# Kernel optimization log

Hardware: AMD Instinct MI355X
Metric: run time of the kernel (lower is better)

## Reference

```python
import jax, jax.numpy as jnp
import numpy as np

EPS = 1e-7
B, F, C, H, W, D = 2, 2, 64, 32, 104, 96


def _pix_homog(h, w):
    ys, xs = jnp.meshgrid(jnp.arange(h, dtype=jnp.float32),
                          jnp.arange(w, dtype=jnp.float32), indexing='ij')
    return jnp.stack([xs.ravel(), ys.ravel(), jnp.ones(h * w, jnp.float32)], 0)  # [3, H*W]


def setup_inputs() -> dict:
    key = jax.random.key(0)
    k1, k2 = jax.random.split(key)
    current_feats = jax.random.normal(k1, (B, C, H, W), jnp.float32)
    lookup_feats = jax.random.normal(k2, (B, F, C, H, W), jnp.float32)

    rng = np.random.RandomState(0)
    # intrinsics at matching (feature) resolution, monodepth2-style
    Km = np.eye(4, dtype=np.float32)
    Km[0, 0] = 0.58 * W
    Km[1, 1] = 1.92 * H
    Km[0, 2] = 0.5 * W
    Km[1, 2] = 0.5 * H
    K = np.tile(Km[None], (B, 1, 1))
    invK = np.linalg.inv(K).astype(np.float32)

    # near-identity relative poses (small rotation perturbation + small translation)
    poses = np.tile(np.eye(4, dtype=np.float32)[None, None], (B, F, 1, 1))
    poses[:, :, :3, :3] += 0.02 * rng.randn(B, F, 3, 3).astype(np.float32)
    poses[:, :, :3, 3] = 0.1 * rng.randn(B, F, 3).astype(np.float32)

    depth_bins = jnp.linspace(0.1, 20.0, D, dtype=jnp.float32)
    return {
        'current_feats': current_feats,
        'lookup_feats': lookup_feats,
        'poses': jnp.asarray(poses),
        'K': jnp.asarray(K),
        'invK': jnp.asarray(invK),
        'depth_bins': depth_bins,
    }


def _grid_sample_zeros(lfT, gx, gy, h, w):
    """Bilinear grid_sample, align_corners=True, padding_mode='zeros'.
    lfT: [B,F,H,W,C]; gx,gy: [B,F,D,H,W] in pixel coords. -> [B,F,D,H,W,C]"""
    x0 = jnp.floor(gx)
    y0 = jnp.floor(gy)
    x0i = x0.astype(jnp.int32)
    y0i = y0.astype(jnp.int32)
    wx1 = gx - x0
    wy1 = gy - y0
    wx0 = 1.0 - wx1
    wy0 = 1.0 - wy1
    bb = jnp.arange(lfT.shape[0])[:, None, None, None, None]
    ff = jnp.arange(lfT.shape[1])[None, :, None, None, None]

    def corner(yi, xi, wgt):
        m = ((xi >= 0) & (xi < w) & (yi >= 0) & (yi < h)).astype(lfT.dtype)
        xc = jnp.clip(xi, 0, w - 1)
        yc = jnp.clip(yi, 0, h - 1)
        v = lfT[bb, ff, yc, xc]                      # [B,F,D,H,W,C]
        return v * (m * wgt)[..., None]

    return (corner(y0i, x0i, wy0 * wx0) + corner(y0i, x0i + 1, wy0 * wx1)
            + corner(y0i + 1, x0i, wy1 * wx0) + corner(y0i + 1, x0i + 1, wy1 * wx1))


def reference(current_feats, lookup_feats, poses, K, invK, depth_bins):
    b, c, h, w = current_feats.shape
    f = lookup_feats.shape[1]
    d = depth_bins.shape[0]

    # Backproject: world points for each hypothesised depth plane
    pix = _pix_homog(h, w)                                   # [3, HW]
    cam = jnp.einsum('bij,jn->bin', invK[:, :3, :3], pix)    # [B,3,HW]
    pts = depth_bins[None, :, None, None] * cam[:, None]     # [B,D,3,HW]
    world = jnp.concatenate([pts, jnp.ones((b, d, 1, h * w), pts.dtype)], 2)  # [B,D,4,HW]

    # Project into each lookup frame
    P = jnp.einsum('bij,bfjk->bfik', K, poses)[:, :, :3, :]  # [B,F,3,4]
    cpts = jnp.einsum('bfij,bdjn->bfdin', P, world)          # [B,F,D,3,HW]
    xy = cpts[:, :, :, :2] / (cpts[:, :, :, 2:3] + EPS)      # pixel coords [B,F,D,2,HW]
    xy = xy.reshape(b, f, d, 2, h, w)
    gx, gy = xy[:, :, :, 0], xy[:, :, :, 1]                  # [B,F,D,H,W]

    # edge mask (detach in original -> stop_gradient)
    sx, sy = jax.lax.stop_gradient(gx), jax.lax.stop_gradient(gy)
    edge = ((sx >= 2.0) & (sx <= w - 2) & (sy >= 2.0) & (sy <= h - 2)).astype(jnp.float32)
    interior = jnp.zeros((h, w), jnp.float32).at[2:-2, 2:-2].set(1.0)
    edge_mask = edge * interior                               # [B,F,D,H,W]

    # warp lookup features and L1-diff against current features
    lfT = lookup_feats.transpose(0, 1, 3, 4, 2)               # [B,F,H,W,C]
    warped = _grid_sample_zeros(lfT, gx, gy, h, w)            # [B,F,D,H,W,C]
    cur = current_feats.transpose(0, 2, 3, 1)                 # [B,H,W,C]
    diffs = jnp.abs(warped - cur[:, None, None]).mean(-1) * edge_mask  # [B,F,D,H,W]

    # skip lookup frames whose pose is all-zero
    valid = (poses.sum((-2, -1)) != 0).astype(jnp.float32)    # [B,F]
    diffs = diffs * valid[:, :, None, None, None]

    cost = diffs.sum(1)                                        # [B,D,H,W]
    counts = (diffs > 0).astype(jnp.float32).sum(1)
    cost = cost / (counts + EPS)

    # set missing values to per-pixel max over depth bins
    missing = (cost == 0.0)
    cmax = cost.max(1, keepdims=True)
    cost = jnp.where(missing, cmax, cost)
    return cost
```

## Files before the change

### kernel.cpp

```cpp
#include <hip/hip_runtime.h>
#include <math.h>

constexpr int B_ = 2, F_ = 2, C_ = 64, H_ = 32, W_ = 104, D_ = 96;
constexpr int HW_ = H_ * W_;
#define EPSF 1e-7f

constexpr size_t LFT_OFF  = 0;
constexpr size_t CURT_OFF = LFT_OFF + (size_t)B_ * F_ * HW_ * C_;

constexpr int NT_BLKS = (HW_ / 32) * (C_ / 32) * (B_ * F_ + B_);
constexpr int DPAD  = D_ + 1;
constexpr int DPADI = D_ + 4;

__global__ __launch_bounds__(256) void prep_kernel(
        const float* __restrict__ cur, const float* __restrict__ lf,
        float* __restrict__ ws) {
    __shared__ float tile[32][33];
    int bid = blockIdx.x;
    int slice = bid / 208;
    int rem   = bid % 208;
    int nb = rem % 104, cb = rem / 104;
    const float* inS;
    float* outS;
    if (slice < B_ * F_) {
        inS  = lf + (size_t)slice * C_ * HW_;
        outS = ws + LFT_OFF + (size_t)slice * HW_ * C_;
    } else {
        int s2 = slice - B_ * F_;
        inS  = cur + (size_t)s2 * C_ * HW_;
        outS = ws + CURT_OFF + (size_t)s2 * HW_ * C_;
    }
    int t = threadIdx.x;
    int tx = t & 31, ty = t >> 5;
    int n0 = nb * 32, c0 = cb * 32;
    #pragma unroll
    for (int k = 0; k < 32; k += 8)
        tile[ty + k][tx] = inS[(size_t)(c0 + ty + k) * HW_ + n0 + tx];
    __syncthreads();
    #pragma unroll
    for (int k = 0; k < 32; k += 8)
        outS[(size_t)(n0 + ty + k) * C_ + c0 + tx] = tile[tx][ty + k];
}

__global__ __launch_bounds__(512, 4) void mega_kernel(
        const float* __restrict__ poses, const float* __restrict__ K,
        const float* __restrict__ invK, const float* __restrict__ depth_bins,
        const float* __restrict__ ws, float* __restrict__ out) {
    int t   = threadIdx.x;
    int bid = blockIdx.x;
    int xt  = bid % 13;  int r = bid / 13;
    int y   = r % H_;
    int b   = r / H_;

    if (y < 2 || y >= H_ - 2) {
        for (int k = t; k < 8 * D_; k += 512) {
            int d = k >> 3, px = k & 7;
            out[((size_t)(b * D_ + d) * H_ + y) * W_ + xt * 8 + px] = 0.0f;
        }
        return;
    }

    __shared__ int    offsL[F_][8][DPADI];
    __shared__ float4 wtsL [F_][8][DPAD];
    __shared__ float  costb[8][DPAD];
    __shared__ float  pmax[32][8];
    __shared__ float  cmaxb[8];

    #pragma unroll
    for (int f = 0; f < F_; ++f) {
        const float* Kb   = K + (size_t)b * 16;
        const float* pose = poses + (size_t)(b * F_ + f) * 16;
        float P[12];
        #pragma unroll
        for (int i = 0; i < 3; ++i) {
            #pragma unroll
            for (int k = 0; k < 4; ++k) {
                float acc = __fmul_rn(Kb[i*4+0], pose[0*4+k]);
                acc = __fmaf_rn(Kb[i*4+1], pose[1*4+k], acc);
                acc = __fmaf_rn(Kb[i*4+2], pose[2*4+k], acc);
                acc = __fmaf_rn(Kb[i*4+3], pose[3*4+k], acc);
                P[i*4+k] = acc;
            }
        }
        float vs = 0.f;
        #pragma unroll
        for (int j = 0; j < 16; ++j) vs += pose[j];
        bool valid = (vs != 0.f);
        const float* iK = invK + (size_t)b * 16;

        #pragma unroll
        for (int k = 0; k < 2; ++k) {
            int idx = t + 512 * k;
            if (idx < 8 * D_) {
                int dd = idx >> 3, px = idx & 7;
                int x = xt * 8 + px;
                float xf = (float)x, yf = (float)y;
                float cam0 = __fmul_rn(iK[0], xf); cam0 = __fmaf_rn(iK[1], yf, cam0); cam0 = __fmaf_rn(iK[2],  1.0f, cam0);
                float cam1 = __fmul_rn(iK[4], xf); cam1 = __fmaf_rn(iK[5], yf, cam1); cam1 = __fmaf_rn(iK[6],  1.0f, cam1);
                float cam2 = __fmul_rn(iK[8], xf); cam2 = __fmaf_rn(iK[9], yf, cam2); cam2 = __fmaf_rn(iK[10], 1.0f, cam2);
                float depth = depth_bins[dd];
                float p0 = __fmul_rn(depth, cam0);
                float p1 = __fmul_rn(depth, cam1);
                float p2 = __fmul_rn(depth, cam2);
                float c0 = __fmul_rn(P[0], p0); c0 = __fmaf_rn(P[1], p1, c0); c0 = __fmaf_rn(P[2],  p2, c0); c0 = __fmaf_rn(P[3],  1.0f, c0);
                float c1 = __fmul_rn(P[4], p0); c1 = __fmaf_rn(P[5], p1, c1); c1 = __fmaf_rn(P[6],  p2, c1); c1 = __fmaf_rn(P[7],  1.0f, c1);
                float c2 = __fmul_rn(P[8], p0); c2 = __fmaf_rn(P[9], p1, c2); c2 = __fmaf_rn(P[10], p2, c2); c2 = __fmaf_rn(P[11], 1.0f, c2);
                float denom = __fadd_rn(c2, EPSF);
                float gx = c0 / denom;
                float gy = c1 / denom;
                bool interior = (x >= 2) && (x <= W_ - 3);
                bool m = valid && interior && (gx >= 2.0f) && (gx <= (float)(W_ - 2))
                                           && (gy >= 2.0f) && (gy <= (float)(H_ - 2));
                if (m) {
                    float x0f = floorf(gx), y0f = floorf(gy);
                    int   x0  = (int)x0f,   y0  = (int)y0f;
                    float wx1 = gx - x0f, wy1 = gy - y0f;
                    float wx0 = 1.f - wx1, wy0 = 1.f - wy1;
                    wtsL[f][px][dd] = make_float4(wy0 * wx0, wy0 * wx1,
                                                  wy1 * wx0, wy1 * wx1);
                    offsL[f][px][dd] = (y0 * W_ + x0) * C_;
                } else {
                    offsL[f][px][dd] = -1;
                    wtsL[f][px][dd] = make_float4(0.f, 0.f, 0.f, 0.f);
                }
            }
        }
    }
    __syncthreads();

    {
        int lane = t & 15, px = (t >> 4) & 7, half = t >> 7;
        int x = xt * 8 + px;
        const float4 cv = *(const float4*)(ws + CURT_OFF
                            + ((size_t)((b * H_ + y) * W_ + x)) * C_ + lane * 4);
        const float* lf0 = ws + LFT_OFF + (size_t)(b * F_ + 0) * HW_ * C_ + lane * 4;
        const float* lf1 = ws + LFT_OFF + (size_t)(b * F_ + 1) * HW_ * C_ + lane * 4;

        float4 cc0[4], cc1[4];
        int oprev0 = -1, oprev1 = -1;
        #pragma unroll
        for (int k = 0; k < 4; ++k)
            cc0[k] = cc1[k] = make_float4(0.f, 0.f, 0.f, 0.f);

        int dbeg = half * (D_ / 4), dend = dbeg + (D_ / 4);
        int    on0 = offsL[0][px][dbeg], on1 = offsL[1][px][dbeg];
        float4 wn0 = wtsL[0][px][dbeg],  wn1 = wtsL[1][px][dbeg];

        for (int dc = dbeg; dc < dend; ++dc) {
            int    oc0 = on0, oc1 = on1;
            float4 wc0 = wn0, wc1 = wn1;
            int nx = (dc + 1 < dend) ? dc + 1 : dc;
            on0 = offsL[0][px][nx]; wn0 = wtsL[0][px][nx];
            on1 = offsL[1][px][nx]; wn1 = wtsL[1][px][nx];

            float costsum = 0.f, counts = 0.f;
            {
                bool m = (oc0 >= 0);
                if (m && oc0 != oprev0) {
                    const float* bp = lf0 + oc0;
                    cc0[0] = *(const float4*)(bp);
                    cc0[1] = *(const float4*)(bp + C_);
                    cc0[2] = *(const float4*)(bp + W_ * C_);
                    cc0[3] = *(const float4*)(bp + W_ * C_ + C_);
                    oprev0 = oc0;
                }
                float s;
                s  = fabsf(cc0[0].x*wc0.x + cc0[1].x*wc0.y + cc0[2].x*wc0.z + cc0[3].x*wc0.w - cv.x);
                s += fabsf(cc0[0].y*wc0.x + cc0[1].y*wc0.y + cc0[2].y*wc0.z + cc0[3].y*wc0.w - cv.y);
                s += fabsf(cc0[0].z*wc0.x + cc0[1].z*wc0.y + cc0[2].z*wc0.z + cc0[3].z*wc0.w - cv.z);
                s += fabsf(cc0[0].w*wc0.x + cc0[1].w*wc0.y + cc0[2].w*wc0.z + cc0[3].w*wc0.w - cv.w);
                s += __shfl_xor(s, 1);
                s += __shfl_xor(s, 2);
                s += __shfl_xor(s, 4);
                s += __shfl_xor(s, 8);
                float diff = __fmul_rn(s, 1.0f / 64.0f) * (m ? 1.0f : 0.0f);
                costsum += diff;
                counts  += (diff > 0.f) ? 1.0f : 0.0f;
            }
            {
                bool m = (oc1 >= 0);
                if (m && oc1 != oprev1) {
                    const float* bp = lf1 + oc1;
                    cc1[0] = *(const float4*)(bp);
                    cc1[1] = *(const float4*)(bp + C_);
                    cc1[2] = *(const float4*)(bp + W_ * C_);
                    cc1[3] = *(const float4*)(bp + W_ * C_ + C_);
                    oprev1 = oc1;
                }
                float s;
                s  = fabsf(cc1[0].x*wc1.x + cc1[1].x*wc1.y + cc1[2].x*wc1.z + cc1[3].x*wc1.w - cv.x);
                s += fabsf(cc1[0].y*wc1.x + cc1[1].y*wc1.y + cc1[2].y*wc1.z + cc1[3].y*wc1.w - cv.y);
                s += fabsf(cc1[0].z*wc1.x + cc1[1].z*wc1.y + cc1[2].z*wc1.z + cc1[3].z*wc1.w - cv.z);
                s += fabsf(cc1[0].w*wc1.x + cc1[1].w*wc1.y + cc1[2].w*wc1.z + cc1[3].w*wc1.w - cv.w);
                s += __shfl_xor(s, 1);
                s += __shfl_xor(s, 2);
                s += __shfl_xor(s, 4);
                s += __shfl_xor(s, 8);
                float diff = __fmul_rn(s, 1.0f / 64.0f) * (m ? 1.0f : 0.0f);
                costsum += diff;
                counts  += (diff > 0.f) ? 1.0f : 0.0f;
            }
            float cost = costsum / __fadd_rn(counts, EPSF);
            if (lane == 0) costb[px][dc] = cost;
        }
    }
    __syncthreads();

    {
        int j = t >> 3, px = t & 7;
        float v[3];
        if (t < 256) {
            float pm = 0.f;
            #pragma unroll
            for (int k = 0; k < 3; ++k) {
                v[k] = costb[px][j + 32 * k];
                pm = fmaxf(pm, v[k]);
            }
            pmax[j][px] = pm;
        }
        __syncthreads();
        if (t < 8) {
            float cm = 0.f;
            #pragma unroll
            for (int jj = 0; jj < 32; ++jj) cm = fmaxf(cm, pmax[jj][t]);
            cmaxb[t] = cm;
        }
        __syncthreads();
        if (t < 256) {
            float cm = cmaxb[px];
            int x = xt * 8 + px;
            #pragma unroll
            for (int k = 0; k < 3; ++k) {
                int d = j + 32 * k;
                out[((size_t)(b * D_ + d) * H_ + y) * W_ + x] = (v[k] == 0.0f) ? cm : v[k];
            }
        }
    }
}

extern "C" void kernel_launch(void* const* d_in, const int* in_sizes, int n_in,
                              void* d_out, int out_size, void* d_ws, size_t ws_size,
                              hipStream_t stream) {
    const float* cur        = (const float*)d_in[0];
    const float* lf         = (const float*)d_in[1];
    const float* poses      = (const float*)d_in[2];
    const float* K          = (const float*)d_in[3];
    const float* invK       = (const float*)d_in[4];
    const float* depth_bins = (const float*)d_in[5];
    float* out = (float*)d_out;
    float* ws  = (float*)d_ws;

    prep_kernel<<<NT_BLKS, 256, 0, stream>>>(cur, lf, ws);
    mega_kernel<<<B_ * H_ * 13, 512, 0, stream>>>(poses, K, invK, depth_bins, ws, out);
}
```

Before: 110.5 us.

## Halve pixels per block and use DPP for 16-lane channel reductions

Each block now covers 4 pixels instead of 8, with 256 threads, so twice as many blocks are launched and occupancy hints are raised. This spreads work more evenly across CUs and adds parallelism on a small grid. The 16-lane shuffle-xor reductions become DPP row operations, which avoids the LDS-permute cost of shuffles. The trade-off is more per-block setup (projection matrix and validity work) repeated across more blocks.

```diff
diff --git a/kernel.cpp b/kernel.cpp
--- a/kernel.cpp
+++ b/kernel.cpp
@@ -9,8 +9,23 @@
 constexpr size_t CURT_OFF = LFT_OFF + (size_t)B_ * F_ * HW_ * C_;
 
 constexpr int NT_BLKS = (HW_ / 32) * (C_ / 32) * (B_ * F_ + B_);
+constexpr int PXB   = 4;
+constexpr int XT_   = W_ / PXB;
 constexpr int DPAD  = D_ + 1;
 constexpr int DPADI = D_ + 4;
+
+template<int CTRL>
+__device__ __forceinline__ float dpp_add(float x) {
+    int y = __builtin_amdgcn_update_dpp(0, __float_as_int(x), CTRL, 0xf, 0xf, true);
+    return x + __int_as_float(y);
+}
+__device__ __forceinline__ float group16_sum(float s) {
+    s = dpp_add<0xB1>(s);
+    s = dpp_add<0x4E>(s);
+    s = dpp_add<0x141>(s);
+    s = dpp_add<0x140>(s);
+    return s;
+}
 
 __global__ __launch_bounds__(256) void prep_kernel(
         const float* __restrict__ cur, const float* __restrict__ lf,
@@ -42,29 +57,29 @@
         outS[(size_t)(n0 + ty + k) * C_ + c0 + tx] = tile[tx][ty + k];
 }
 
-__global__ __launch_bounds__(512, 4) void mega_kernel(
+__global__ __launch_bounds__(256, 6) void mega_kernel(
         const float* __restrict__ poses, const float* __restrict__ K,
         const float* __restrict__ invK, const float* __restrict__ depth_bins,
         const float* __restrict__ ws, float* __restrict__ out) {
     int t   = threadIdx.x;
     int bid = blockIdx.x;
-    int xt  = bid % 13;  int r = bid / 13;
+    int xt  = bid % XT_;  int r = bid / XT_;
     int y   = r % H_;
     int b   = r / H_;
 
     if (y < 2 || y >= H_ - 2) {
-        for (int k = t; k < 8 * D_; k += 512) {
-            int d = k >> 3, px = k & 7;
-            out[((size_t)(b * D_ + d) * H_ + y) * W_ + xt * 8 + px] = 0.0f;
+        for (int k = t; k < PXB * D_; k += 256) {
+            int d = k >> 2, px = k & 3;
+            out[((size_t)(b * D_ + d) * H_ + y) * W_ + xt * PXB + px] = 0.0f;
         }
         return;
     }
 
-    __shared__ int    offsL[F_][8][DPADI];
-    __shared__ float4 wtsL [F_][8][DPAD];
-    __shared__ float  costb[8][DPAD];
-    __shared__ float  pmax[32][8];
-    __shared__ float  cmaxb[8];
+    __shared__ int    offsL[F_][PXB][DPADI];
+    __shared__ float4 wtsL [F_][PXB][DPAD];
+    __shared__ float  costb[PXB][DPAD];
+    __shared__ float  pmax[32][PXB];
+    __shared__ float  cmaxb[PXB];
 
     #pragma unroll
     for (int f = 0; f < F_; ++f) {
@@ -90,10 +105,10 @@
 
         #pragma unroll
         for (int k = 0; k < 2; ++k) {
-            int idx = t + 512 * k;
-            if (idx < 8 * D_) {
-                int dd = idx >> 3, px = idx & 7;
-                int x = xt * 8 + px;
+            int idx = t + 256 * k;
+            if (idx < PXB * D_) {
+                int dd = idx >> 2, px = idx & 3;
+                int x = xt * PXB + px;
                 float xf = (float)x, yf = (float)y;
                 float cam0 = __fmul_rn(iK[0], xf); cam0 = __fmaf_rn(iK[1], yf, cam0); cam0 = __fmaf_rn(iK[2],  1.0f, cam0);
                 float cam1 = __fmul_rn(iK[4], xf); cam1 = __fmaf_rn(iK[5], yf, cam1); cam1 = __fmaf_rn(iK[6],  1.0f, cam1);
@@ -129,8 +144,8 @@
     __syncthreads();
 
     {
-        int lane = t & 15, px = (t >> 4) & 7, half = t >> 7;
-        int x = xt * 8 + px;
+        int lane = t & 15, px = (t >> 4) & 3, half = t >> 6;
+        int x = xt * PXB + px;
         const float4 cv = *(const float4*)(ws + CURT_OFF
                             + ((size_t)((b * H_ + y) * W_ + x)) * C_ + lane * 4);
         const float* lf0 = ws + LFT_OFF + (size_t)(b * F_ + 0) * HW_ * C_ + lane * 4;
@@ -169,10 +184,7 @@
                 s += fabsf(cc0[0].y*wc0.x + cc0[1].y*wc0.y + cc0[2].y*wc0.z + cc0[3].y*wc0.w - cv.y);
                 s += fabsf(cc0[0].z*wc0.x + cc0[1].z*wc0.y + cc0[2].z*wc0.z + cc0[3].z*wc0.w - cv.z);
                 s += fabsf(cc0[0].w*wc0.x + cc0[1].w*wc0.y + cc0[2].w*wc0.z + cc0[3].w*wc0.w - cv.w);
-                s += __shfl_xor(s, 1);
-                s += __shfl_xor(s, 2);
-                s += __shfl_xor(s, 4);
-                s += __shfl_xor(s, 8);
+                s = group16_sum(s);
                 float diff = __fmul_rn(s, 1.0f / 64.0f) * (m ? 1.0f : 0.0f);
                 costsum += diff;
                 counts  += (diff > 0.f) ? 1.0f : 0.0f;
@@ -192,10 +204,7 @@
                 s += fabsf(cc1[0].y*wc1.x + cc1[1].y*wc1.y + cc1[2].y*wc1.z + cc1[3].y*wc1.w - cv.y);
                 s += fabsf(cc1[0].z*wc1.x + cc1[1].z*wc1.y + cc1[2].z*wc1.z + cc1[3].z*wc1.w - cv.z);
                 s += fabsf(cc1[0].w*wc1.x + cc1[1].w*wc1.y + cc1[2].w*wc1.z + cc1[3].w*wc1.w - cv.w);
-                s += __shfl_xor(s, 1);
-                s += __shfl_xor(s, 2);
-                s += __shfl_xor(s, 4);
-                s += __shfl_xor(s, 8);
+                s = group16_sum(s);
                 float diff = __fmul_rn(s, 1.0f / 64.0f) * (m ? 1.0f : 0.0f);
                 costsum += diff;
                 counts  += (diff > 0.f) ? 1.0f : 0.0f;
@@ -207,9 +216,9 @@
     __syncthreads();
 
     {
-        int j = t >> 3, px = t & 7;
+        int j = t >> 2, px = t & 3;
         float v[3];
-        if (t < 256) {
+        if (t < 128) {
             float pm = 0.f;
             #pragma unroll
             for (int k = 0; k < 3; ++k) {
@@ -219,16 +228,16 @@
             pmax[j][px] = pm;
         }
         __syncthreads();
-        if (t < 8) {
+        if (t < PXB) {
             float cm = 0.f;
             #pragma unroll
             for (int jj = 0; jj < 32; ++jj) cm = fmaxf(cm, pmax[jj][t]);
             cmaxb[t] = cm;
         }
         __syncthreads();
-        if (t < 256) {
+        if (t < 128) {
             float cm = cmaxb[px];
-            int x = xt * 8 + px;
+            int x = xt * PXB + px;
             #pragma unroll
             for (int k = 0; k < 3; ++k) {
                 int d = j + 32 * k;
@@ -251,5 +260,5 @@
     float* ws  = (float*)d_ws;
 
     prep_kernel<<<NT_BLKS, 256, 0, stream>>>(cur, lf, ws);
-    mega_kernel<<<B_ * H_ * 13, 512, 0, stream>>>(poses, K, invK, depth_bins, ws, out);
-}
+    mega_kernel<<<B_ * H_ * XT_, 256, 0, stream>>>(poses, K, invK, depth_bins, ws, out);
+}
```

New measurement: 100.9 us. 1.1x faster.
